# Performance work log

Hardware: AMD Instinct MI355X
Metric: run time of the kernel (lower is better)

Reference implementation:

```python
import jax, jax.numpy as jnp
import numpy as np

B, N, H = 4, 256, 512
P = 128  # game_physics_params


def _init(key, shape, scale=0.02):
    return jax.random.normal(key, shape, dtype=jnp.float32) * scale


def setup_inputs() -> dict:
    key = jax.random.key(0)
    ks = jax.random.split(key, 16)
    return {
        "object_features": jax.random.normal(ks[0], (B, N, H), dtype=jnp.float32),
        # physics_predictor: H -> 512 -> P
        "pp_w1": _init(ks[1], (H, 512)), "pp_b1": jnp.zeros((512,), jnp.float32),
        "pp_w2": _init(ks[2], (512, P)), "pp_b2": jnp.zeros((P,), jnp.float32),
        # collision_detector: 2H -> 256 -> 128 -> 1
        "cd_w1": _init(ks[3], (2 * H, 256)), "cd_b1": jnp.zeros((256,), jnp.float32),
        "cd_w2": _init(ks[4], (256, 128)), "cd_b2": jnp.zeros((128,), jnp.float32),
        "cd_w3": _init(ks[5], (128, 1)), "cd_b3": jnp.zeros((1,), jnp.float32),
        # velocity / force heads: H -> 3
        "vel_w": _init(ks[6], (H, 3)), "vel_b": jnp.zeros((3,), jnp.float32),
        "frc_w": _init(ks[7], (H, 3)), "frc_b": jnp.zeros((3,), jnp.float32),
    }


def reference(object_features, pp_w1, pp_b1, pp_w2, pp_b2,
              cd_w1, cd_b1, cd_w2, cd_b2, cd_w3, cd_b3,
              vel_w, vel_b, frc_w, frc_b):
    x = object_features  # [B, N, H]
    # physics predictor MLP
    p = jax.nn.relu(x @ pp_w1 + pp_b1) @ pp_w2 + pp_b2  # [B, N, P]
    mass = jax.nn.sigmoid(p[..., 0:1]) * 100.0
    friction = jax.nn.sigmoid(p[..., 1:2])
    elasticity = jax.nn.sigmoid(p[..., 2:3])
    density = jax.nn.sigmoid(p[..., 3:4]) * 10.0
    velocities = x @ vel_w + vel_b  # [B, N, 3]
    forces = x @ frc_w + frc_b      # [B, N, 3]

    # vectorized pairwise collision detection over upper-triangle pairs
    iu, ju = np.triu_indices(N, k=1)  # static index arrays, length Np = N(N-1)/2
    pairs = jnp.concatenate([x[:, iu], x[:, ju]], axis=-1)  # [B, Np, 2H]
    h = jax.nn.relu(pairs @ cd_w1 + cd_b1)
    h = jax.nn.relu(h @ cd_w2 + cd_b2)
    prob = jax.nn.sigmoid(h @ cd_w3 + cd_b3)[..., 0]  # [B, Np]
    collision_matrix = jnp.zeros((x.shape[0], N, N), dtype=x.dtype)
    collision_matrix = collision_matrix.at[:, iu, ju].set(prob).at[:, ju, iu].set(prob)

    return (mass, friction, elasticity, density, velocities, forces, collision_matrix)
```

## Files before the change

### kernel.cpp

```cpp
#include <hip/hip_runtime.h>
#include <hip/hip_bf16.h>

typedef __attribute__((ext_vector_type(8))) short bf16x8;
typedef __attribute__((ext_vector_type(4))) float f32x4;

__device__ __forceinline__ float sigmoidf_(float v) {
    return 1.0f / (1.0f + __expf(-v));
}
__device__ __forceinline__ short f2bf(float f) {
    union { __hip_bfloat16 h; short s; } cv;
    cv.h = __float2bfloat16(f);
    return cv.s;
}
__device__ __forceinline__ float bf2f(short s) {
    union { float f; unsigned u; } cv;
    cv.u = ((unsigned)(unsigned short)s) << 16;
    return cv.f;
}

__global__ __launch_bounds__(256) void convert_kernel(
    const float* __restrict__ x, const float* __restrict__ pp_w1,
    const float* __restrict__ cd_w1, const float* __restrict__ cd_w2,
    const float* __restrict__ pp_w2, const float* __restrict__ vel_w,
    const float* __restrict__ frc_w,
    __hip_bfloat16* __restrict__ xb, __hip_bfloat16* __restrict__ Wt,
    __hip_bfloat16* __restrict__ w2t, float* __restrict__ hw)
{
    __shared__ float ts[64][65];
    const int b = blockIdx.x, t = threadIdx.x;

    if (b < 256) {
        int base = b * 2048 + t * 8;
        float4 a = *(const float4*)(x + base);
        float4 c = *(const float4*)(x + base + 4);
        bf16x8 o;
        o[0] = f2bf(a.x); o[1] = f2bf(a.y); o[2] = f2bf(a.z); o[3] = f2bf(a.w);
        o[4] = f2bf(c.x); o[5] = f2bf(c.y); o[6] = f2bf(c.z); o[7] = f2bf(c.w);
        *(bf16x8*)(xb + base) = o;
        return;
    }
    if (b == 392) {
        for (int e = t; e < 5120; e += 256) {
            int h = e >> 9, k = e & 511;
            float v = (h < 4) ? pp_w2[k * 128 + h]
                    : (h < 7) ? vel_w[k * 3 + (h - 4)]
                              : frc_w[k * 3 + (h - 7)];
            hw[e] = v;
        }
        return;
    }

    const float* src; int ss, k0, n0, region;
    if (b < 320)      { int i = b - 256; src = pp_w1; ss = 512; k0 = (i >> 3) * 64; n0 = (i & 7) * 64; region = 0; }
    else if (b < 384) { int i = b - 320; src = cd_w1; ss = 256; k0 = (i >> 2) * 64; n0 = (i & 3) * 64; region = 1; }
    else              { int i = b - 384; src = cd_w2; ss = 128; k0 = (i >> 1) * 64; n0 = (i & 1) * 64; region = 2; }

    #pragma unroll
    for (int i = 0; i < 4; ++i) {
        int r = (t >> 4) + i * 16, c4 = (t & 15) * 4;
        *(float4*)&ts[r][c4] = *(const float4*)(src + (k0 + r) * ss + n0 + c4);
    }
    __syncthreads();
    #pragma unroll
    for (int i = 0; i < 4; ++i) {
        int nOut = (t >> 4) + i * 16, kc = (t & 15) * 4;
        ushort4 o;
        o.x = (unsigned short)f2bf(ts[kc + 0][nOut]);
        o.y = (unsigned short)f2bf(ts[kc + 1][nOut]);
        o.z = (unsigned short)f2bf(ts[kc + 2][nOut]);
        o.w = (unsigned short)f2bf(ts[kc + 3][nOut]);
        int gn = n0 + nOut, gk = k0 + kc;
        if (region == 0)      *(ushort4*)(Wt + gn * 512 + gk) = o;
        else if (region == 1) {
            int row = (gk < 512) ? (512 + gn) : (768 + gn);
            *(ushort4*)(Wt + row * 512 + (gk & 511)) = o;
        } else                *(ushort4*)(w2t + gn * 256 + gk) = o;
    }
}

__global__ __launch_bounds__(256) void gemm_kernel(
    const __hip_bfloat16* __restrict__ xb, const __hip_bfloat16* __restrict__ Wt,
    const float* __restrict__ pp_b1, const float* __restrict__ cd_b1,
    __hip_bfloat16* __restrict__ hidg, __hip_bfloat16* __restrict__ Ugb,
    __hip_bfloat16* __restrict__ Vgb)
{
    const int t = threadIdx.x;
    const int wave = t >> 6, lane = t & 63;
    const int l = lane & 15, q = lane >> 4;
    const int m0 = blockIdx.y * 32;
    const int n0 = blockIdx.x * 128 + wave * 32;

    const __hip_bfloat16* a0p = xb + (m0 + l) * 512 + q * 8;
    const __hip_bfloat16* a1p = a0p + 16 * 512;
    const __hip_bfloat16* b0p = Wt + (n0 + l) * 512 + q * 8;
    const __hip_bfloat16* b1p = b0p + 16 * 512;

    f32x4 acc00 = {}, acc01 = {}, acc10 = {}, acc11 = {};
    #pragma unroll
    for (int ks = 0; ks < 16; ++ks) {
        bf16x8 a0 = *(const bf16x8*)(a0p + ks * 32);
        bf16x8 a1 = *(const bf16x8*)(a1p + ks * 32);
        bf16x8 b0 = *(const bf16x8*)(b0p + ks * 32);
        bf16x8 b1 = *(const bf16x8*)(b1p + ks * 32);
        acc00 = __builtin_amdgcn_mfma_f32_16x16x32_bf16(a0, b0, acc00, 0, 0, 0);
        acc01 = __builtin_amdgcn_mfma_f32_16x16x32_bf16(a0, b1, acc01, 0, 0, 0);
        acc10 = __builtin_amdgcn_mfma_f32_16x16x32_bf16(a1, b0, acc10, 0, 0, 0);
        acc11 = __builtin_amdgcn_mfma_f32_16x16x32_bf16(a1, b1, acc11, 0, 0, 0);
    }

    const int c0 = n0 + l, c1 = n0 + 16 + l;
    #pragma unroll
    for (int mt = 0; mt < 2; ++mt) {
        const f32x4& A0 = mt ? acc10 : acc00;
        const f32x4& A1 = mt ? acc11 : acc01;
        if (n0 < 512) {
            float b0v = pp_b1[c0], b1v = pp_b1[c1];
            #pragma unroll
            for (int r = 0; r < 4; ++r) {
                int rg = m0 + mt * 16 + q * 4 + r;
                hidg[rg * 512 + c0] = __float2bfloat16(fmaxf(A0[r] + b0v, 0.f));
                hidg[rg * 512 + c1] = __float2bfloat16(fmaxf(A1[r] + b1v, 0.f));
            }
        } else if (n0 < 768) {
            float b0v = cd_b1[c0 - 512], b1v = cd_b1[c1 - 512];
            #pragma unroll
            for (int r = 0; r < 4; ++r) {
                int rg = m0 + mt * 16 + q * 4 + r;
                Ugb[rg * 256 + (c0 - 512)] = __float2bfloat16(A0[r] + b0v);
                Ugb[rg * 256 + (c1 - 512)] = __float2bfloat16(A1[r] + b1v);
            }
        } else {
            #pragma unroll
            for (int r = 0; r < 4; ++r) {
                int rg = m0 + mt * 16 + q * 4 + r;
                Vgb[rg * 256 + (c0 - 768)] = __float2bfloat16(A0[r]);
                Vgb[rg * 256 + (c1 - 768)] = __float2bfloat16(A1[r]);
            }
        }
    }
}

__global__ __launch_bounds__(256, 2) void pair_kernel(
    const __hip_bfloat16* __restrict__ Ugb, const __hip_bfloat16* __restrict__ Vgb,
    const __hip_bfloat16* __restrict__ w2t,
    const float* __restrict__ cd_b2, const float* __restrict__ cd_w3,
    const float* __restrict__ cd_b3, float* __restrict__ cm,
    const float* __restrict__ x, const __hip_bfloat16* __restrict__ hidg,
    const float* __restrict__ hw, const float* __restrict__ pp_b2,
    const float* __restrict__ vel_b, const float* __restrict__ frc_b,
    float* __restrict__ out)
{
    __shared__ __align__(16) char smem[35840];

    const int t = threadIdx.x;
    const int wave = t >> 6, lane = t & 63;
    const int bx = blockIdx.x;

    if (bx >= 1056) {
        float* hwl = (float*)smem;
        #pragma unroll
        for (int i = 0; i < 5; ++i) {
            int idx = i * 256 + t;
            ((float4*)hwl)[idx] = ((const float4*)hw)[idx];
        }
        __syncthreads();

        const int row0 = (bx - 1056) * 8 + wave * 2;
        const float4* xr0 = (const float4*)(x + row0 * 512);
        const float4* xr1 = (const float4*)(x + (row0 + 1) * 512);
        float4 xa0 = xr0[lane * 2], xc0 = xr0[lane * 2 + 1];
        float4 xa1 = xr1[lane * 2], xc1 = xr1[lane * 2 + 1];
        bf16x8 hb0 = *(const bf16x8*)(hidg + row0 * 512 + lane * 8);
        bf16x8 hb1 = *(const bf16x8*)(hidg + (row0 + 1) * 512 + lane * 8);

        #pragma unroll
        for (int rr = 0; rr < 2; ++rr) {
            const int row = row0 + rr;
            float4 xa = rr ? xa1 : xa0, xc = rr ? xc1 : xc0;
            bf16x8 hb = rr ? hb1 : hb0;
            float hf[8];
            #pragma unroll
            for (int j = 0; j < 8; ++j) hf[j] = bf2f(hb[j]);

            #pragma unroll
            for (int h = 0; h < 10; ++h) {
                const float4* wr = (const float4*)(hwl + h * 512);
                float4 wa = wr[lane * 2], wc = wr[lane * 2 + 1];
                float s;
                if (h < 4) {
                    s = hf[0]*wa.x + hf[1]*wa.y + hf[2]*wa.z + hf[3]*wa.w
                      + hf[4]*wc.x + hf[5]*wc.y + hf[6]*wc.z + hf[7]*wc.w;
                } else {
                    s = xa.x*wa.x + xa.y*wa.y + xa.z*wa.z + xa.w*wa.w
                      + xc.x*wc.x + xc.y*wc.y + xc.z*wc.z + xc.w*wc.w;
                }
                s += __shfl_xor(s, 1);  s += __shfl_xor(s, 2);
                s += __shfl_xor(s, 4);  s += __shfl_xor(s, 8);
                s += __shfl_xor(s, 16); s += __shfl_xor(s, 32);
                if (lane == 0) {
                    if (h < 4) {
                        float sg = sigmoidf_(s + pp_b2[h]);
                        out[h * 1024 + row] = (h == 0) ? sg * 100.f : (h == 3) ? sg * 10.f : sg;
                    } else if (h < 7) {
                        out[4096 + row * 3 + (h - 4)] = s + vel_b[h - 4];
                    } else {
                        out[7168 + row * 3 + (h - 7)] = s + frc_b[h - 7];
                    }
                }
            }
        }
        return;
    }

    char* rawBB = smem;
    char* hsB   = smem + 16384;
    float (*ps)[64][4] = (float (*)[64][4])(smem + 16384 + 17408);

    const int tp = bx >> 1;
    const int ub = (bx & 1) << 1;
    int ti = (int)((65.0f - sqrtf(4225.0f - 8.0f * (float)tp)) * 0.5f);
    while ((ti + 1) * (65 - (ti + 1)) / 2 <= tp) ++ti;
    while (ti * (65 - ti) / 2 > tp) --ti;
    const int tj = ti + (tp - ti * (65 - ti) / 2);
    const int i0 = ti * 8, j0 = tj * 8;

    const int l = lane & 15, q = lane >> 4;

    const __hip_bfloat16* wb0 = w2t + ((wave * 2 + 0) * 16 + l) * 256 + q * 8;
    const __hip_bfloat16* wb1 = wb0 + 16 * 256;
    bf16x8 w2r0[8], w2r1[8];
    __builtin_amdgcn_sched_barrier(0);
    #pragma unroll
    for (int ks = 0; ks < 8; ++ks) {
        asm volatile("global_load_dwordx4 %0, %1, off"
                     : "=&v"(w2r0[ks]) : "v"(wb0 + ks * 32));
        asm volatile("global_load_dwordx4 %0, %1, off"
                     : "=&v"(w2r1[ks]) : "v"(wb1 + ks * 32));
    }
    __builtin_amdgcn_sched_barrier(0);

    const float b2v0 = cd_b2[(wave * 2 + 0) * 16 + l];
    const float b2v1 = cd_b2[(wave * 2 + 1) * 16 + l];
    const float w3v0 = cd_w3[(wave * 2 + 0) * 16 + l];
    const float w3v1 = cd_w3[(wave * 2 + 1) * 16 + l];
    const float b3 = cd_b3[0];

    __builtin_amdgcn_sched_barrier(0);
    {
        const int r0 = wave * 2;
        const int rlane = r0 + (lane >> 5);
        const int slot = lane & 31;
        const int gk16 = slot ^ (rlane & 7);
        #pragma unroll
        for (int ul = 0; ul < 2; ++ul) {
            const int u = ub + ul;
            const __hip_bfloat16* us = Ugb + ((u << 8) + i0 + rlane) * 256 + gk16 * 8;
            const __hip_bfloat16* vs = Vgb + ((u << 8) + j0 + rlane) * 256 + gk16 * 8;
            char* du = rawBB + (((ul << 1) + 0) * 8 + r0) * 512;
            char* dv = rawBB + (((ul << 1) + 1) * 8 + r0) * 512;
            __builtin_amdgcn_global_load_lds(
                (const __attribute__((address_space(1))) void*)us,
                (__attribute__((address_space(3))) void*)du, 16, 0, 0);
            __builtin_amdgcn_global_load_lds(
                (const __attribute__((address_space(1))) void*)vs,
                (__attribute__((address_space(3))) void*)dv, 16, 0, 0);
        }
    }
    __builtin_amdgcn_sched_barrier(0);

    f32x4 acc[4][2];

    const int ur = lane >> 3, vr = lane & 7;
    auto CVT = [&](int ul, int h) {
        const char* RU = rawBB + ((ul << 1) + 0) * 4096;
        const char* RV = rawBB + ((ul << 1) + 1) * 4096;
        #pragma unroll
        for (int i = 0; i < 4; ++i) {
            const int s16 = (wave << 2) + i;
            const int gs = (h << 4) + s16;
            bf16x8 ubv = *(const bf16x8*)(RU + ur * 512 + ((gs ^ ur) << 4));
            bf16x8 vbv = *(const bf16x8*)(RV + vr * 512 + ((gs ^ vr) << 4));
            bf16x8 o;
            #pragma unroll
            for (int j = 0; j < 8; ++j)
                o[j] = f2bf(fmaxf(bf2f(ubv[j]) + bf2f(vbv[j]), 0.f));
            *(bf16x8*)(hsB + s16 * 1088 + lane * 16) = o;
        }
    };
    auto MFMAH = [&](int h) {
        #pragma unroll
        for (int ks = 0; ks < 4; ++ks) {
            bf16x8 bfr0 = w2r0[h * 4 + ks];
            bf16x8 bfr1 = w2r1[h * 4 + ks];
            #pragma unroll
            for (int mt = 0; mt < 4; ++mt) {
                bf16x8 afr = *(const bf16x8*)(hsB + (ks * 4 + q) * 1088 + (mt * 16 + l) * 16);
                acc[mt][0] = __builtin_amdgcn_mfma_f32_16x16x32_bf16(afr, bfr0, acc[mt][0], 0, 0, 0);
                acc[mt][1] = __builtin_amdgcn_mfma_f32_16x16x32_bf16(afr, bfr1, acc[mt][1], 0, 0, 0);
            }
        }
    };
    auto EPI = [&](int u) {
        #pragma unroll
        for (int mt = 0; mt < 4; ++mt) {
            #pragma unroll
            for (int r = 0; r < 4; ++r) {
                float g0 = fmaxf(acc[mt][0][r] + b2v0, 0.f);
                float g1 = fmaxf(acc[mt][1][r] + b2v1, 0.f);
                float s = g0 * w3v0 + g1 * w3v1;
                s += __shfl_xor(s, 1);
                s += __shfl_xor(s, 2);
                s += __shfl_xor(s, 4);
                s += __shfl_xor(s, 8);
                if (l == 0) ps[u & 1][mt * 16 + q * 4 + r][wave] = s;
            }
        }
    };
    auto FIN = [&](int u) {
        if (t < 64) {
            int p = t;
            float v = ps[u & 1][p][0] + ps[u & 1][p][1] + ps[u & 1][p][2]
                    + ps[u & 1][p][3] + b3;
            float prob = 1.0f / (1.0f + __expf(-v));
            int i = i0 + (p >> 3), j = j0 + (p & 7);
            float* base = cm + u * 65536;
            if (i < j) {
                base[i * 256 + j] = prob;
                base[j * 256 + i] = prob;
            } else if (i == j) {
                base[i * 256 + i] = 0.0f;
            }
        }
    };

    #pragma unroll
    for (int ul = 0; ul < 2; ++ul) {
        if (ul == 0) asm volatile("s_waitcnt vmcnt(2) lgkmcnt(0)" ::: "memory");
        else         asm volatile("s_waitcnt vmcnt(0) lgkmcnt(0)" ::: "memory");
        __builtin_amdgcn_s_barrier();
        __builtin_amdgcn_sched_barrier(0);

        #pragma unroll
        for (int mt = 0; mt < 4; ++mt) {
            acc[mt][0] = (f32x4){0.f, 0.f, 0.f, 0.f};
            acc[mt][1] = (f32x4){0.f, 0.f, 0.f, 0.f};
        }

        CVT(ul, 0);
        if (ul == 1) FIN(ub);
        asm volatile("s_waitcnt lgkmcnt(0)" ::: "memory");
        __builtin_amdgcn_s_barrier();
        __builtin_amdgcn_sched_barrier(0);

        MFMAH(0);
        __builtin_amdgcn_s_barrier();
        __builtin_amdgcn_sched_barrier(0);

        CVT(ul, 1);
        asm volatile("s_waitcnt lgkmcnt(0)" ::: "memory");
        __builtin_amdgcn_s_barrier();
        __builtin_amdgcn_sched_barrier(0);

        MFMAH(1);
        EPI(ub + ul);
    }
    asm volatile("s_waitcnt lgkmcnt(0)" ::: "memory");
    __builtin_amdgcn_s_barrier();
    FIN(ub + 1);
}

extern "C" void kernel_launch(void* const* d_in, const int* in_sizes, int n_in,
                              void* d_out, int out_size, void* d_ws, size_t ws_size,
                              hipStream_t stream) {
    const float* x     = (const float*)d_in[0];
    const float* pp_w1 = (const float*)d_in[1];
    const float* pp_b1 = (const float*)d_in[2];
    const float* pp_w2 = (const float*)d_in[3];
    const float* pp_b2 = (const float*)d_in[4];
    const float* cd_w1 = (const float*)d_in[5];
    const float* cd_b1 = (const float*)d_in[6];
    const float* cd_w2 = (const float*)d_in[7];
    const float* cd_b2 = (const float*)d_in[8];
    const float* cd_w3 = (const float*)d_in[9];
    const float* cd_b3 = (const float*)d_in[10];
    const float* vel_w = (const float*)d_in[11];
    const float* vel_b = (const float*)d_in[12];
    const float* frc_w = (const float*)d_in[13];
    const float* frc_b = (const float*)d_in[14];

    float* out = (float*)d_out;
    __hip_bfloat16* Ugb  = (__hip_bfloat16*)d_ws;
    __hip_bfloat16* Vgb  = Ugb + 262144;
    __hip_bfloat16* xb   = Vgb + 262144;
    __hip_bfloat16* Wt   = xb + 524288;
    __hip_bfloat16* hidg = Wt + 524288;
    __hip_bfloat16* w2t  = hidg + 524288;
    float* hw = (float*)(w2t + 32768);

    convert_kernel<<<dim3(393), dim3(256), 0, stream>>>(
        x, pp_w1, cd_w1, cd_w2, pp_w2, vel_w, frc_w, xb, Wt, w2t, hw);
    gemm_kernel<<<dim3(8, 32), dim3(256), 0, stream>>>(
        xb, Wt, pp_b1, cd_b1, hidg, Ugb, Vgb);
    pair_kernel<<<dim3(1184), dim3(256), 0, stream>>>(
        Ugb, Vgb, w2t, cd_b2, cd_w3, cd_b3, out + 10240,
        x, hidg, hw, pp_b2, vel_b, frc_b, out);
}
```

Measured before the change: 133.6 us.

## Make pair kernel persistent with double-buffered tile loads across work items

Result: slower. 153.2 us (+14.7%).

```diff
diff --git a/kernel.cpp b/kernel.cpp
--- a/kernel.cpp
+++ b/kernel.cpp
@@ -156,7 +156,7 @@
     const int wave = t >> 6, lane = t & 63;
     const int bx = blockIdx.x;
 
-    if (bx >= 1056) {
+    if (bx >= 224) {
         float* hwl = (float*)smem;
         #pragma unroll
         for (int i = 0; i < 5; ++i) {
@@ -165,46 +165,50 @@
         }
         __syncthreads();
 
-        const int row0 = (bx - 1056) * 8 + wave * 2;
-        const float4* xr0 = (const float4*)(x + row0 * 512);
-        const float4* xr1 = (const float4*)(x + (row0 + 1) * 512);
-        float4 xa0 = xr0[lane * 2], xc0 = xr0[lane * 2 + 1];
-        float4 xa1 = xr1[lane * 2], xc1 = xr1[lane * 2 + 1];
-        bf16x8 hb0 = *(const bf16x8*)(hidg + row0 * 512 + lane * 8);
-        bf16x8 hb1 = *(const bf16x8*)(hidg + (row0 + 1) * 512 + lane * 8);
-
-        #pragma unroll
-        for (int rr = 0; rr < 2; ++rr) {
-            const int row = row0 + rr;
-            float4 xa = rr ? xa1 : xa0, xc = rr ? xc1 : xc0;
-            bf16x8 hb = rr ? hb1 : hb0;
-            float hf[8];
-            #pragma unroll
-            for (int j = 0; j < 8; ++j) hf[j] = bf2f(hb[j]);
-
-            #pragma unroll
-            for (int h = 0; h < 10; ++h) {
-                const float4* wr = (const float4*)(hwl + h * 512);
-                float4 wa = wr[lane * 2], wc = wr[lane * 2 + 1];
-                float s;
-                if (h < 4) {
-                    s = hf[0]*wa.x + hf[1]*wa.y + hf[2]*wa.z + hf[3]*wa.w
-                      + hf[4]*wc.x + hf[5]*wc.y + hf[6]*wc.z + hf[7]*wc.w;
-                } else {
-                    s = xa.x*wa.x + xa.y*wa.y + xa.z*wa.z + xa.w*wa.w
-                      + xc.x*wc.x + xc.y*wc.y + xc.z*wc.z + xc.w*wc.w;
-                }
-                s += __shfl_xor(s, 1);  s += __shfl_xor(s, 2);
-                s += __shfl_xor(s, 4);  s += __shfl_xor(s, 8);
-                s += __shfl_xor(s, 16); s += __shfl_xor(s, 32);
-                if (lane == 0) {
+        const int rbase = (bx - 224) * 32;
+        #pragma unroll
+        for (int pass = 0; pass < 4; ++pass) {
+            const int row0 = rbase + pass * 8 + wave * 2;
+            const float4* xr0 = (const float4*)(x + row0 * 512);
+            const float4* xr1 = (const float4*)(x + (row0 + 1) * 512);
+            float4 xa0 = xr0[lane * 2], xc0 = xr0[lane * 2 + 1];
+            float4 xa1 = xr1[lane * 2], xc1 = xr1[lane * 2 + 1];
+            bf16x8 hb0 = *(const bf16x8*)(hidg + row0 * 512 + lane * 8);
+            bf16x8 hb1 = *(const bf16x8*)(hidg + (row0 + 1) * 512 + lane * 8);
+
+            #pragma unroll
+            for (int rr = 0; rr < 2; ++rr) {
+                const int row = row0 + rr;
+                float4 xa = rr ? xa1 : xa0, xc = rr ? xc1 : xc0;
+                bf16x8 hb = rr ? hb1 : hb0;
+                float hf[8];
+                #pragma unroll
+                for (int j = 0; j < 8; ++j) hf[j] = bf2f(hb[j]);
+
+                #pragma unroll
+                for (int h = 0; h < 10; ++h) {
+                    const float4* wr = (const float4*)(hwl + h * 512);
+                    float4 wa = wr[lane * 2], wc = wr[lane * 2 + 1];
+                    float s;
                     if (h < 4) {
-                        float sg = sigmoidf_(s + pp_b2[h]);
-                        out[h * 1024 + row] = (h == 0) ? sg * 100.f : (h == 3) ? sg * 10.f : sg;
-                    } else if (h < 7) {
-                        out[4096 + row * 3 + (h - 4)] = s + vel_b[h - 4];
+                        s = hf[0]*wa.x + hf[1]*wa.y + hf[2]*wa.z + hf[3]*wa.w
+                          + hf[4]*wc.x + hf[5]*wc.y + hf[6]*wc.z + hf[7]*wc.w;
                     } else {
-                        out[7168 + row * 3 + (h - 7)] = s + frc_b[h - 7];
+                        s = xa.x*wa.x + xa.y*wa.y + xa.z*wa.z + xa.w*wa.w
+                          + xc.x*wc.x + xc.y*wc.y + xc.z*wc.z + xc.w*wc.w;
+                    }
+                    s += __shfl_xor(s, 1);  s += __shfl_xor(s, 2);
+                    s += __shfl_xor(s, 4);  s += __shfl_xor(s, 8);
+                    s += __shfl_xor(s, 16); s += __shfl_xor(s, 32);
+                    if (lane == 0) {
+                        if (h < 4) {
+                            float sg = sigmoidf_(s + pp_b2[h]);
+                            out[h * 1024 + row] = (h == 0) ? sg * 100.f : (h == 3) ? sg * 10.f : sg;
+                        } else if (h < 7) {
+                            out[4096 + row * 3 + (h - 4)] = s + vel_b[h - 4];
+                        } else {
+                            out[7168 + row * 3 + (h - 7)] = s + frc_b[h - 7];
+                        }
                     }
                 }
             }
@@ -212,23 +216,19 @@
         return;
     }
 
-    char* rawBB = smem;
-    char* hsB   = smem + 16384;
-    float (*ps)[64][4] = (float (*)[64][4])(smem + 16384 + 17408);
-
-    const int tp = bx >> 1;
-    const int ub = (bx & 1) << 1;
-    int ti = (int)((65.0f - sqrtf(4225.0f - 8.0f * (float)tp)) * 0.5f);
-    while ((ti + 1) * (65 - (ti + 1)) / 2 <= tp) ++ti;
-    while (ti * (65 - ti) / 2 > tp) --ti;
-    const int tj = ti + (tp - ti * (65 - ti) / 2);
-    const int i0 = ti * 8, j0 = tj * 8;
+    char* rawB = smem;
+    char* hsB  = smem + 16384;
+    float (*ps)[64][4] = (float (*)[64][4])(smem + 33792);
+
+    const int nU = (bx < 96) ? 10 : 9;
+    const int e0 = (bx < 96) ? bx * 10 : 960 + (bx - 96) * 9;
 
     const int l = lane & 15, q = lane >> 4;
 
     const __hip_bfloat16* wb0 = w2t + ((wave * 2 + 0) * 16 + l) * 256 + q * 8;
     const __hip_bfloat16* wb1 = wb0 + 16 * 256;
     bf16x8 w2r0[8], w2r1[8];
+    float b2v0, b2v1, w3v0, w3v1, b3;
     __builtin_amdgcn_sched_barrier(0);
     #pragma unroll
     for (int ks = 0; ks < 8; ++ks) {
@@ -237,43 +237,51 @@
         asm volatile("global_load_dwordx4 %0, %1, off"
                      : "=&v"(w2r1[ks]) : "v"(wb1 + ks * 32));
     }
+    asm volatile("global_load_dword %0, %1, off" : "=&v"(b2v0) : "v"(cd_b2 + (wave * 2 + 0) * 16 + l));
+    asm volatile("global_load_dword %0, %1, off" : "=&v"(b2v1) : "v"(cd_b2 + (wave * 2 + 1) * 16 + l));
+    asm volatile("global_load_dword %0, %1, off" : "=&v"(w3v0) : "v"(cd_w3 + (wave * 2 + 0) * 16 + l));
+    asm volatile("global_load_dword %0, %1, off" : "=&v"(w3v1) : "v"(cd_w3 + (wave * 2 + 1) * 16 + l));
+    asm volatile("global_load_dword %0, %1, off" : "=&v"(b3)   : "v"(cd_b3));
     __builtin_amdgcn_sched_barrier(0);
 
-    const float b2v0 = cd_b2[(wave * 2 + 0) * 16 + l];
-    const float b2v1 = cd_b2[(wave * 2 + 1) * 16 + l];
-    const float w3v0 = cd_w3[(wave * 2 + 0) * 16 + l];
-    const float w3v1 = cd_w3[(wave * 2 + 1) * 16 + l];
-    const float b3 = cd_b3[0];
+    const int r0 = wave * 2;
+    const int rlane = r0 + (lane >> 5);
+    const int slot = lane & 31;
+    const int gk16 = slot ^ (rlane & 7);
+
+    auto DECODE = [&](int e, int& i0_, int& j0_, int& u_) {
+        int tp = e >> 2; u_ = e & 3;
+        int ti = (int)((65.0f - sqrtf(4225.0f - 8.0f * (float)tp)) * 0.5f);
+        while ((ti + 1) * (65 - (ti + 1)) / 2 <= tp) ++ti;
+        while (ti * (65 - ti) / 2 > tp) --ti;
+        int tj = ti + (tp - ti * (65 - ti) / 2);
+        i0_ = ti * 8; j0_ = tj * 8;
+    };
+    auto ISSUE = [&](int e, int buf) {
+        int i0_, j0_, u_;
+        DECODE(e, i0_, j0_, u_);
+        const __hip_bfloat16* us = Ugb + ((u_ << 8) + i0_ + rlane) * 256 + gk16 * 8;
+        const __hip_bfloat16* vs = Vgb + ((u_ << 8) + j0_ + rlane) * 256 + gk16 * 8;
+        char* du = rawB + buf * 8192 + 0 * 4096 + r0 * 512;
+        char* dv = rawB + buf * 8192 + 1 * 4096 + r0 * 512;
+        __builtin_amdgcn_global_load_lds(
+            (const __attribute__((address_space(1))) void*)us,
+            (__attribute__((address_space(3))) void*)du, 16, 0, 0);
+        __builtin_amdgcn_global_load_lds(
+            (const __attribute__((address_space(1))) void*)vs,
+            (__attribute__((address_space(3))) void*)dv, 16, 0, 0);
+    };
 
     __builtin_amdgcn_sched_barrier(0);
-    {
-        const int r0 = wave * 2;
-        const int rlane = r0 + (lane >> 5);
-        const int slot = lane & 31;
-        const int gk16 = slot ^ (rlane & 7);
-        #pragma unroll
-        for (int ul = 0; ul < 2; ++ul) {
-            const int u = ub + ul;
-            const __hip_bfloat16* us = Ugb + ((u << 8) + i0 + rlane) * 256 + gk16 * 8;
-            const __hip_bfloat16* vs = Vgb + ((u << 8) + j0 + rlane) * 256 + gk16 * 8;
-            char* du = rawBB + (((ul << 1) + 0) * 8 + r0) * 512;
-            char* dv = rawBB + (((ul << 1) + 1) * 8 + r0) * 512;
-            __builtin_amdgcn_global_load_lds(
-                (const __attribute__((address_space(1))) void*)us,
-                (__attribute__((address_space(3))) void*)du, 16, 0, 0);
-            __builtin_amdgcn_global_load_lds(
-                (const __attribute__((address_space(1))) void*)vs,
-                (__attribute__((address_space(3))) void*)dv, 16, 0, 0);
-        }
-    }
+    ISSUE(e0, 0);
     __builtin_amdgcn_sched_barrier(0);
 
     f32x4 acc[4][2];
-
     const int ur = lane >> 3, vr = lane & 7;
-    auto CVT = [&](int ul, int h) {
-        const char* RU = rawBB + ((ul << 1) + 0) * 4096;
-        const char* RV = rawBB + ((ul << 1) + 1) * 4096;
+
+    auto CVT = [&](int buf, int h) {
+        const char* RU = rawB + buf * 8192;
+        const char* RV = RU + 4096;
         #pragma unroll
         for (int i = 0; i < 4; ++i) {
             const int s16 = (wave << 2) + i;
@@ -300,7 +308,7 @@
             }
         }
     };
-    auto EPI = [&](int u) {
+    auto EPI = [&](int par) {
         #pragma unroll
         for (int mt = 0; mt < 4; ++mt) {
             #pragma unroll
@@ -312,18 +320,18 @@
                 s += __shfl_xor(s, 2);
                 s += __shfl_xor(s, 4);
                 s += __shfl_xor(s, 8);
-                if (l == 0) ps[u & 1][mt * 16 + q * 4 + r][wave] = s;
-            }
-        }
-    };
-    auto FIN = [&](int u) {
+                if (l == 0) ps[par][mt * 16 + q * 4 + r][wave] = s;
+            }
+        }
+    };
+    auto FIN = [&](int fi0, int fj0, int fu, int par) {
         if (t < 64) {
             int p = t;
-            float v = ps[u & 1][p][0] + ps[u & 1][p][1] + ps[u & 1][p][2]
-                    + ps[u & 1][p][3] + b3;
+            float v = ps[par][p][0] + ps[par][p][1] + ps[par][p][2]
+                    + ps[par][p][3] + b3;
             float prob = 1.0f / (1.0f + __expf(-v));
-            int i = i0 + (p >> 3), j = j0 + (p & 7);
-            float* base = cm + u * 65536;
+            int i = fi0 + (p >> 3), j = fj0 + (p & 7);
+            float* base = cm + fu * 65536;
             if (i < j) {
                 base[i * 256 + j] = prob;
                 base[j * 256 + i] = prob;
@@ -333,10 +341,18 @@
         }
     };
 
-    #pragma unroll
-    for (int ul = 0; ul < 2; ++ul) {
-        if (ul == 0) asm volatile("s_waitcnt vmcnt(2) lgkmcnt(0)" ::: "memory");
-        else         asm volatile("s_waitcnt vmcnt(0) lgkmcnt(0)" ::: "memory");
+    int pi0 = 0, pj0 = 0, pu = 0;
+    #pragma unroll 1
+    for (int idx = 0; idx < nU; ++idx) {
+        int ci0, cj0, cu;
+        DECODE(e0 + idx, ci0, cj0, cu);
+
+        if (idx + 1 < nU) {
+            ISSUE(e0 + idx + 1, (idx + 1) & 1);
+            asm volatile("s_waitcnt vmcnt(2) lgkmcnt(0)" ::: "memory");
+        } else {
+            asm volatile("s_waitcnt vmcnt(0) lgkmcnt(0)" ::: "memory");
+        }
         __builtin_amdgcn_s_barrier();
         __builtin_amdgcn_sched_barrier(0);
 
@@ -346,8 +362,8 @@
             acc[mt][1] = (f32x4){0.f, 0.f, 0.f, 0.f};
         }
 
-        CVT(ul, 0);
-        if (ul == 1) FIN(ub);
+        CVT(idx & 1, 0);
+        if (idx > 0) FIN(pi0, pj0, pu, (idx - 1) & 1);
         asm volatile("s_waitcnt lgkmcnt(0)" ::: "memory");
         __builtin_amdgcn_s_barrier();
         __builtin_amdgcn_sched_barrier(0);
@@ -356,17 +372,18 @@
         __builtin_amdgcn_s_barrier();
         __builtin_amdgcn_sched_barrier(0);
 
-        CVT(ul, 1);
+        CVT(idx & 1, 1);
         asm volatile("s_waitcnt lgkmcnt(0)" ::: "memory");
         __builtin_amdgcn_s_barrier();
         __builtin_amdgcn_sched_barrier(0);
 
         MFMAH(1);
-        EPI(ub + ul);
+        EPI(idx & 1);
+        pi0 = ci0; pj0 = cj0; pu = cu;
     }
     asm volatile("s_waitcnt lgkmcnt(0)" ::: "memory");
     __builtin_amdgcn_s_barrier();
-    FIN(ub + 1);
+    FIN(pi0, pj0, pu, (nU - 1) & 1);
 }
 
 extern "C" void kernel_launch(void* const* d_in, const int* in_sizes, int n_in,
@@ -401,7 +418,7 @@
         x, pp_w1, cd_w1, cd_w2, pp_w2, vel_w, frc_w, xb, Wt, w2t, hw);
     gemm_kernel<<<dim3(8, 32), dim3(256), 0, stream>>>(
         xb, Wt, pp_b1, cd_b1, hidg, Ugb, Vgb);
-    pair_kernel<<<dim3(1184), dim3(256), 0, stream>>>(
+    pair_kernel<<<dim3(256), dim3(256), 0, stream>>>(
         Ugb, Vgb, w2t, cd_b2, cd_w3, cd_b3, out + 10240,
         x, hidg, hw, pp_b2, vel_b, frc_b, out);
 }
```
